# Kernel tuning notes

Measured on AMD Instinct MI355X. Metric: run time of the kernel, lower is better.

Reference implementation:

```python
import jax, jax.numpy as jnp
import numpy as np

N = 50000          # nodes
E = 800000         # edges (before self-loops)
F_IN = 128         # num_features
HEADS = 4
OUT = 128 // HEADS # per-head channels = num_hidden // heads
NEG_SLOPE = 0.2    # PyG GATConv default


def setup_inputs() -> dict:
    key = jax.random.key(0)
    ks = jax.random.split(key, 10)
    x = jax.random.normal(ks[0], (N, F_IN), jnp.float32)
    edge_index = jax.random.randint(ks[1], (2, E), 0, N, dtype=jnp.int64)
    sW = 1.0 / np.sqrt(F_IN)
    sA = 1.0 / np.sqrt(OUT)
    return {
        "x": x,
        "edge_index": edge_index,
        "W1": jax.random.normal(ks[2], (F_IN, HEADS * OUT), jnp.float32) * sW,
        "a_src1": jax.random.normal(ks[3], (HEADS, OUT), jnp.float32) * sA,
        "a_dst1": jax.random.normal(ks[4], (HEADS, OUT), jnp.float32) * sA,
        "b1": jnp.zeros((HEADS * OUT,), jnp.float32),
        "W2": jax.random.normal(ks[5], (HEADS * OUT, HEADS * OUT), jnp.float32) * sW,
        "a_src2": jax.random.normal(ks[6], (HEADS, OUT), jnp.float32) * sA,
        "a_dst2": jax.random.normal(ks[7], (HEADS, OUT), jnp.float32) * sA,
        "b2": jnp.zeros((HEADS * OUT,), jnp.float32),
    }


def gat_conv(x, src, dst, W, a_src, a_dst, b):
    """One GATConv layer (PyG semantics, concat heads, self-loops already in src/dst)."""
    n = x.shape[0]
    h = (x @ W).reshape(n, HEADS, OUT)                 # [N, H, C]
    # per-node attention halves, gathered per edge -> [Etot, H]
    alpha = (h * a_src).sum(-1)[src] + (h * a_dst).sum(-1)[dst]
    alpha = jax.nn.leaky_relu(alpha, NEG_SLOPE)
    # softmax over incoming edges of each destination node (stable)
    amax = jax.ops.segment_max(alpha, dst, num_segments=n)
    ex = jnp.exp(alpha - amax[dst])
    denom = jax.ops.segment_sum(ex, dst, num_segments=n)
    attn = ex / (denom[dst] + 1e-16)                    # [Etot, H]
    # weighted message scatter-add
    out = jax.ops.segment_sum(h[src] * attn[..., None], dst, num_segments=n)
    return out.reshape(n, HEADS * OUT) + b


def reference(x, edge_index, W1, a_src1, a_dst1, b1, W2, a_src2, a_dst2, b2):
    loops = jnp.arange(N, dtype=edge_index.dtype)       # PyG add_self_loops=True
    src = jnp.concatenate([edge_index[0], loops])
    dst = jnp.concatenate([edge_index[1], loops])
    h = jax.nn.relu(gat_conv(x, src, dst, W1, a_src1, a_dst1, b1))
    # dropout = identity in eval mode
    h = jax.nn.relu(gat_conv(h, src, dst, W2, a_src2, a_dst2, b2))
    return h
```

## Files before the change

kernel.cpp:

```cpp
#include <hip/hip_runtime.h>
#include <hip/hip_fp16.h>
#include <cstdint>
#include <cstddef>

#define NN 50000
#define EE 800000
#define ETOT (EE + NN)
#define FD 128
#define NH 4
#define NEG_SLOPE 0.2f

#define BSHIFT 10
#define BSIZE 1024
#define NBKT ((NN + BSIZE - 1) / BSIZE)
#define CAPG 20000
#define CHUNK 2048
#define P1_BLOCKS ((ETOT + CHUNK - 1) / CHUNK)

typedef _Float16 half8 __attribute__((ext_vector_type(8)));
typedef float f32x4 __attribute__((ext_vector_type(4)));


__global__ void zero_kernel(int* __restrict__ gcnt) {
    int t = threadIdx.x;
    if (t < NBKT) gcnt[t] = 0;
}


__global__ __launch_bounds__(256) void bin_kernel(const int* __restrict__ ei,
                                                  int* __restrict__ gcnt,
                                                  uint32_t* __restrict__ gbkt,
                                                  const float* __restrict__ W1,
                                                  const float* __restrict__ W2,
                                                  uint4* __restrict__ Wf1,
                                                  uint4* __restrict__ Wf2) {
    if (blockIdx.x >= P1_BLOCKS) {
        const float* W = (blockIdx.x - P1_BLOCKS) ? W2 : W1;
        uint4* Wf = (blockIdx.x - P1_BLOCKS) ? Wf2 : Wf1;
        for (int s = threadIdx.x; s < 2048; s += 256) {
            int fi = s >> 6;
            int lane = s & 63;
            int ct = fi >> 2, ks = fi & 3;
            int col = ct * 16 + (lane & 15);
            int kb = ks * 32 + (lane >> 4) * 8;
            half8 h;
            #pragma unroll
            for (int j = 0; j < 8; ++j) h[j] = (_Float16)W[(kb + j) * FD + col];
            Wf[s] = *(uint4*)&h;
        }
        return;
    }
    __shared__ int lcnt[NBKT];
    __shared__ int gb[NBKT];
    const int t = threadIdx.x;
    if (t < NBKT) lcnt[t] = 0;
    __syncthreads();
    const int base = blockIdx.x * CHUNK;
    uint32_t pk[8]; int bk[8]; int sl[8];
    #pragma unroll
    for (int j = 0; j < 8; ++j) {
        int e = base + j * 256 + t;
        bk[j] = -1;
        if (e < ETOT) {
            int src, dst;
            if (e < EE) { src = ei[e]; dst = ei[EE + e]; }
            else        { src = e - EE; dst = src; }
            int b = dst >> BSHIFT;
            bk[j] = b;
            pk[j] = (uint32_t)src | ((uint32_t)(dst & (BSIZE - 1)) << 16);
            sl[j] = atomicAdd(&lcnt[b], 1);
        }
    }
    __syncthreads();
    if (t < NBKT) gb[t] = atomicAdd(&gcnt[t], lcnt[t]);
    __syncthreads();
    #pragma unroll
    for (int j = 0; j < 8; ++j)
        if (bk[j] >= 0)
            gbkt[(size_t)bk[j] * CAPG + gb[bk[j]] + sl[j]] = pk[j];
}


__global__ __launch_bounds__(1024) void sort_kernel(const int* __restrict__ gcnt,
                                                    const uint32_t* __restrict__ gbkt,
                                                    int* __restrict__ row_ptr,
                                                    int* __restrict__ csr) {
    __shared__ int cnt[BSIZE];
    __shared__ int pfx[BSIZE];
    __shared__ int wsum[16];
    __shared__ int sCbase;
    const int b = blockIdx.x;
    const int t = threadIdx.x;
    const int count = gcnt[b];
    const int dstBase = b << BSHIFT;
    const int ndst = (NN - dstBase < BSIZE) ? (NN - dstBase) : BSIZE;
    const uint32_t* mybkt = gbkt + (size_t)b * CAPG;
    cnt[t] = 0;
    if (t < 64) {
        int v = (t < NBKT) ? gcnt[t] : 0;
        int inc = v;
        #pragma unroll
        for (int off = 1; off < 64; off <<= 1) {
            int u = __shfl_up(inc, off);
            if (t >= off) inc += u;
        }
        if (t == b) sCbase = inc - v;
    }
    __syncthreads();
    const int cbase = sCbase;
    for (int i = t; i < count; i += 1024)
        atomicAdd(&cnt[mybkt[i] >> 16], 1);
    __syncthreads();
    int v = cnt[t];
    int inc = v;
    const int lane = t & 63, wid = t >> 6;
    #pragma unroll
    for (int off = 1; off < 64; off <<= 1) {
        int u = __shfl_up(inc, off);
        if (lane >= off) inc += u;
    }
    if (lane == 63) wsum[wid] = inc;
    __syncthreads();
    if (t < 16) {
        int w = wsum[t]; int wi = w;
        #pragma unroll
        for (int off = 1; off < 16; off <<= 1) {
            int u = __shfl_up(wi, off);
            if (t >= off) wi += u;
        }
        wsum[t] = wi - w;
    }
    __syncthreads();
    int excl = wsum[wid] + inc - v;
    pfx[t] = excl;
    if (t < ndst) row_ptr[dstBase + t] = cbase + excl;
    if (b == NBKT - 1 && t == 0) row_ptr[NN] = ETOT;
    cnt[t] = 0;
    __syncthreads();
    for (int i = t; i < count; i += 1024) {
        uint32_t pkv = mybkt[i];
        int dl = pkv >> 16;
        int r = atomicAdd(&cnt[dl], 1);
        csr[cbase + pfx[dl] + r] = (int)(pkv & 0xFFFFu);
    }
}


__global__ __launch_bounds__(256) void gemm_kernel(const float* __restrict__ X,
                                                   const uint4* __restrict__ Wf,
                                                   __half* __restrict__ Hh) {
    const int tid = threadIdx.x;
    const int wv = tid >> 6, lane = tid & 63;
    const int l15 = lane & 15, lg = lane >> 4;
    const int rowA = blockIdx.x * 64 + wv * 16 + l15;
    const int rA = (rowA < NN) ? rowA : NN - 1;
    half8 a[4];
    #pragma unroll
    for (int ks = 0; ks < 4; ++ks) {
        int kb = ks * 32 + lg * 8;
        float4 x0 = *(const float4*)&X[(size_t)rA * FD + kb];
        float4 x1 = *(const float4*)&X[(size_t)rA * FD + kb + 4];
        a[ks][0] = (_Float16)x0.x; a[ks][1] = (_Float16)x0.y;
        a[ks][2] = (_Float16)x0.z; a[ks][3] = (_Float16)x0.w;
        a[ks][4] = (_Float16)x1.x; a[ks][5] = (_Float16)x1.y;
        a[ks][6] = (_Float16)x1.z; a[ks][7] = (_Float16)x1.w;
    }
    const int rowC = blockIdx.x * 64 + wv * 16 + lg * 4;
    #pragma unroll
    for (int ct = 0; ct < 8; ++ct) {
        uint4 braw[4];
        #pragma unroll
        for (int ks = 0; ks < 4; ++ks) braw[ks] = Wf[(ct * 4 + ks) * 64 + lane];
        f32x4 acc = {0.f, 0.f, 0.f, 0.f};
        #pragma unroll
        for (int ks = 0; ks < 4; ++ks) {
            half8 b = *(half8*)&braw[ks];
            acc = __builtin_amdgcn_mfma_f32_16x16x32_f16(a[ks], b, acc, 0, 0, 0);
        }
        #pragma unroll
        for (int r = 0; r < 4; ++r) {
            int gr = rowC + r;
            if (gr < NN) Hh[(size_t)gr * FD + ct * 16 + l15] = __float2half(acc[r]);
        }
    }
}


__global__ __launch_bounds__(256) void adot_kernel(const __half* __restrict__ H,
                                                   const float* __restrict__ a_src,
                                                   const float* __restrict__ a_dst,
                                                   float* __restrict__ AS,
                                                   float* __restrict__ AD) {
    int gt = blockIdx.x * 256 + threadIdx.x;
    int n = gt >> 4;
    int l = gt & 15;
    if (n >= NN) return;
    union { uint4 u; __half2 q[4]; } hv;
    hv.u = *(const uint4*)&H[(size_t)n * FD + l * 8];
    float ps = 0.f, pd = 0.f;
    #pragma unroll
    for (int j = 0; j < 4; ++j) {
        float2 f = __half22float2(hv.q[j]);
        ps += f.x * a_src[l * 8 + 2 * j] + f.y * a_src[l * 8 + 2 * j + 1];
        pd += f.x * a_dst[l * 8 + 2 * j] + f.y * a_dst[l * 8 + 2 * j + 1];
    }
    ps += __shfl_xor(ps, 1); ps += __shfl_xor(ps, 2);
    pd += __shfl_xor(pd, 1); pd += __shfl_xor(pd, 2);
    if ((l & 3) == 0) {
        AS[n * NH + (l >> 2)] = ps;
        AD[n * NH + (l >> 2)] = pd;
    }
}


__device__ __forceinline__ float sel4(float a0, float a1, float a2, float a3, int h) {
    float lo = (h & 1) ? a1 : a0;
    float hi = (h & 1) ? a3 : a2;
    return (h & 2) ? hi : lo;
}

__global__ __launch_bounds__(256) void agg_kernel(const __half* __restrict__ H,
                                                  const float* __restrict__ AS,
                                                  const float* __restrict__ AD,
                                                  const int* __restrict__ row_ptr,
                                                  const int* __restrict__ csr_src,
                                                  const float* __restrict__ bias,
                                                  float* __restrict__ Out) {
    __shared__ float sP[8][32][5];
    __shared__ int   sS[8][32];
    const int wave = threadIdx.x >> 6;
    const int lane = threadIdx.x & 63;
    const int sub  = lane >> 5;
    const int sl   = lane & 31;
    const int ws   = wave * 2 + sub;
    const int n = blockIdx.x * 8 + ws;
    const int start = row_ptr[n], end = row_ptr[n + 1];
    const int h0 = sl >> 3;
    const float4 adv = *(const float4*)&AD[n * NH];
    float s[NH] = {0.f, 0.f, 0.f, 0.f};
    float acc0 = 0.f, acc1 = 0.f, acc2 = 0.f, acc3 = 0.f;

    for (int base = start; base < end; base += 32) {
        int cn = end - base; if (cn > 32) cn = 32;
        int my_src = 0;
        float al[NH];
        if (sl < cn) {
            my_src = csr_src[base + sl];
            float4 asv = *(const float4*)&AS[my_src * NH];
            al[0] = asv.x + adv.x; al[1] = asv.y + adv.y;
            al[2] = asv.z + adv.z; al[3] = asv.w + adv.w;
        }
        sS[ws][sl] = my_src;
        #pragma unroll
        for (int h = 0; h < NH; ++h) {
            float aa = al[h];
            aa = (aa > 0.f) ? aa : NEG_SLOPE * aa;
            float pp = (sl < cn) ? __expf(aa) : 0.f;
            sP[ws][sl][h] = pp;
            #pragma unroll
            for (int off = 16; off; off >>= 1) pp += __shfl_xor(pp, off, 32);
            s[h] += pp;
        }
        #pragma unroll 4
        for (int e = 0; e < cn; ++e) {
            float pm = sP[ws][e][h0];
            int se = sS[ws][e];
            union { uint2 u; __half2 q[2]; } hv;
            hv.u = *(const uint2*)&H[(size_t)se * FD + sl * 4];
            float2 f0 = __half22float2(hv.q[0]);
            float2 f1 = __half22float2(hv.q[1]);
            acc0 += pm * f0.x; acc1 += pm * f0.y;
            acc2 += pm * f1.x; acc3 += pm * f1.y;
        }
    }
    float sh = sel4(s[0], s[1], s[2], s[3], h0);
    float inv = 1.f / (sh + 1e-16f);
    const float4 bv = *(const float4*)&bias[sl * 4];
    float4 ov;
    ov.x = fmaxf(acc0 * inv + bv.x, 0.f);
    ov.y = fmaxf(acc1 * inv + bv.y, 0.f);
    ov.z = fmaxf(acc2 * inv + bv.z, 0.f);
    ov.w = fmaxf(acc3 * inv + bv.w, 0.f);
    *(float4*)&Out[(size_t)n * FD + sl * 4] = ov;
}


extern "C" void kernel_launch(void* const* d_in, const int* in_sizes, int n_in,
                              void* d_out, int out_size, void* d_ws, size_t ws_size,
                              hipStream_t stream) {
    const float* x     = (const float*)d_in[0];
    const int*   ei    = (const int*)d_in[1];
    const float* W1    = (const float*)d_in[2];
    const float* asrc1 = (const float*)d_in[3];
    const float* adst1 = (const float*)d_in[4];
    const float* b1    = (const float*)d_in[5];
    const float* W2    = (const float*)d_in[6];
    const float* asrc2 = (const float*)d_in[7];
    const float* adst2 = (const float*)d_in[8];
    const float* b2    = (const float*)d_in[9];
    float* out = (float*)d_out;

    char* p = (char*)d_ws;
    auto alloc = [&](size_t bytes) {
        char* q = p;
        p += (bytes + 255) & ~(size_t)255;
        return q;
    };
    int*      row_ptr = (int*)alloc((NN + 1) * sizeof(int));
    int*      gcnt    = (int*)alloc(NBKT * sizeof(int));
    uint32_t* gbkt    = (uint32_t*)alloc((size_t)NBKT * CAPG * sizeof(uint32_t));
    int*      csr     = (int*)alloc((size_t)ETOT * sizeof(int));
    float*    AS      = (float*)alloc((size_t)NN * NH * sizeof(float));
    float*    AD      = (float*)alloc((size_t)NN * NH * sizeof(float));
    __half*   Hh      = (__half*)alloc((size_t)NN * FD * sizeof(__half));
    uint4*    Wf1     = (uint4*)alloc(2048 * sizeof(uint4));
    uint4*    Wf2     = (uint4*)alloc(2048 * sizeof(uint4));
    (void)ws_size; (void)in_sizes; (void)n_in; (void)out_size;

    zero_kernel<<<1, 64, 0, stream>>>(gcnt);
    bin_kernel<<<P1_BLOCKS + 2, 256, 0, stream>>>(ei, gcnt, gbkt, W1, W2, Wf1, Wf2);
    sort_kernel<<<NBKT, 1024, 0, stream>>>(gcnt, gbkt, row_ptr, csr);

    gemm_kernel<<<(NN + 63) / 64, 256, 0, stream>>>(x, Wf1, Hh);
    adot_kernel<<<(NN * 16 + 255) / 256, 256, 0, stream>>>(Hh, asrc1, adst1, AS, AD);
    agg_kernel<<<NN / 8, 256, 0, stream>>>(Hh, AS, AD, row_ptr, csr, b1, out);

    gemm_kernel<<<(NN + 63) / 64, 256, 0, stream>>>(out, Wf2, Hh);
    adot_kernel<<<(NN * 16 + 255) / 256, 256, 0, stream>>>(Hh, asrc2, adst2, AS, AD);
    agg_kernel<<<NN / 8, 256, 0, stream>>>(Hh, AS, AD, row_ptr, csr, b2, out);
}
```

Before: 150.3 us.

## Process four edges per wave concurrently with 16-byte feature loads in aggregation

The aggregation kernel now assigns one full 64-lane wave per destination node instead of a half-wave. Lanes are split into four edge slots of 16 lanes, and each lane loads 8 half-precision channels (16 bytes) per edge. Partial sums are combined across edge slots with cross-lane shuffles at the end. The intent is more memory-level parallelism and wider loads in the gather loop. The cost is extra shuffle reductions, idle lanes at low-degree tails, and half as many nodes per block.

```diff
diff --git a/kernel.cpp b/kernel.cpp
--- a/kernel.cpp
+++ b/kernel.cpp
@@ -213,12 +213,6 @@
 }
 
 
-__device__ __forceinline__ float sel4(float a0, float a1, float a2, float a3, int h) {
-    float lo = (h & 1) ? a1 : a0;
-    float hi = (h & 1) ? a3 : a2;
-    return (h & 2) ? hi : lo;
-}
-
 __global__ __launch_bounds__(256) void agg_kernel(const __half* __restrict__ H,
                                                   const float* __restrict__ AS,
                                                   const float* __restrict__ AD,
@@ -226,62 +220,77 @@
                                                   const int* __restrict__ csr_src,
                                                   const float* __restrict__ bias,
                                                   float* __restrict__ Out) {
-    __shared__ float sP[8][32][5];
-    __shared__ int   sS[8][32];
-    const int wave = threadIdx.x >> 6;
+    __shared__ float sP[4][64][5];
+    __shared__ int   sS[4][64];
+    const int wv   = threadIdx.x >> 6;
     const int lane = threadIdx.x & 63;
-    const int sub  = lane >> 5;
-    const int sl   = lane & 31;
-    const int ws   = wave * 2 + sub;
-    const int n = blockIdx.x * 8 + ws;
+    const int n = blockIdx.x * 4 + wv;
     const int start = row_ptr[n], end = row_ptr[n + 1];
-    const int h0 = sl >> 3;
+    const int eslot = lane >> 4;
+    const int c8    = lane & 15;
+    const int hme   = c8 >> 2;
     const float4 adv = *(const float4*)&AD[n * NH];
     float s[NH] = {0.f, 0.f, 0.f, 0.f};
-    float acc0 = 0.f, acc1 = 0.f, acc2 = 0.f, acc3 = 0.f;
-
-    for (int base = start; base < end; base += 32) {
-        int cn = end - base; if (cn > 32) cn = 32;
+    float acc[8] = {0.f, 0.f, 0.f, 0.f, 0.f, 0.f, 0.f, 0.f};
+
+    for (int base = start; base < end; base += 64) {
+        int cn = end - base; if (cn > 64) cn = 64;
         int my_src = 0;
         float al[NH];
-        if (sl < cn) {
-            my_src = csr_src[base + sl];
+        if (lane < cn) {
+            my_src = csr_src[base + lane];
             float4 asv = *(const float4*)&AS[my_src * NH];
             al[0] = asv.x + adv.x; al[1] = asv.y + adv.y;
             al[2] = asv.z + adv.z; al[3] = asv.w + adv.w;
         }
-        sS[ws][sl] = my_src;
+        sS[wv][lane] = my_src;
         #pragma unroll
         for (int h = 0; h < NH; ++h) {
             float aa = al[h];
             aa = (aa > 0.f) ? aa : NEG_SLOPE * aa;
-            float pp = (sl < cn) ? __expf(aa) : 0.f;
-            sP[ws][sl][h] = pp;
+            float pp = (lane < cn) ? __expf(aa) : 0.f;
+            sP[wv][lane][h] = pp;
             #pragma unroll
-            for (int off = 16; off; off >>= 1) pp += __shfl_xor(pp, off, 32);
+            for (int off = 32; off; off >>= 1) pp += __shfl_xor(pp, off);
             s[h] += pp;
         }
-        #pragma unroll 4
-        for (int e = 0; e < cn; ++e) {
-            float pm = sP[ws][e][h0];
-            int se = sS[ws][e];
-            union { uint2 u; __half2 q[2]; } hv;
-            hv.u = *(const uint2*)&H[(size_t)se * FD + sl * 4];
-            float2 f0 = __half22float2(hv.q[0]);
-            float2 f1 = __half22float2(hv.q[1]);
-            acc0 += pm * f0.x; acc1 += pm * f0.y;
-            acc2 += pm * f1.x; acc3 += pm * f1.y;
-        }
-    }
-    float sh = sel4(s[0], s[1], s[2], s[3], h0);
-    float inv = 1.f / (sh + 1e-16f);
-    const float4 bv = *(const float4*)&bias[sl * 4];
-    float4 ov;
-    ov.x = fmaxf(acc0 * inv + bv.x, 0.f);
-    ov.y = fmaxf(acc1 * inv + bv.y, 0.f);
-    ov.z = fmaxf(acc2 * inv + bv.z, 0.f);
-    ov.w = fmaxf(acc3 * inv + bv.w, 0.f);
-    *(float4*)&Out[(size_t)n * FD + sl * 4] = ov;
+        #pragma unroll 2
+        for (int cb = 0; cb < cn; cb += 4) {
+            int e = cb + eslot;
+            if (e < cn) {
+                int   se = sS[wv][e];
+                float pm = sP[wv][e][hme];
+                union { uint4 u; __half2 q[4]; } hv;
+                hv.u = *(const uint4*)&H[(size_t)se * FD + c8 * 8];
+                #pragma unroll
+                for (int j = 0; j < 4; ++j) {
+                    float2 f = __half22float2(hv.q[j]);
+                    acc[2 * j]     += pm * f.x;
+                    acc[2 * j + 1] += pm * f.y;
+                }
+            }
+        }
+    }
+    #pragma unroll
+    for (int m = 16; m <= 32; m <<= 1)
+        #pragma unroll
+        for (int j = 0; j < 8; ++j) acc[j] += __shfl_xor(acc[j], m);
+    if (eslot == 0) {
+        float inv = 1.f / (s[hme] + 1e-16f);
+        float4 b0 = *(const float4*)&bias[c8 * 8];
+        float4 b1 = *(const float4*)&bias[c8 * 8 + 4];
+        float4 o0, o1;
+        o0.x = fmaxf(acc[0] * inv + b0.x, 0.f);
+        o0.y = fmaxf(acc[1] * inv + b0.y, 0.f);
+        o0.z = fmaxf(acc[2] * inv + b0.z, 0.f);
+        o0.w = fmaxf(acc[3] * inv + b0.w, 0.f);
+        o1.x = fmaxf(acc[4] * inv + b1.x, 0.f);
+        o1.y = fmaxf(acc[5] * inv + b1.y, 0.f);
+        o1.z = fmaxf(acc[6] * inv + b1.z, 0.f);
+        o1.w = fmaxf(acc[7] * inv + b1.w, 0.f);
+        *(float4*)&Out[(size_t)n * FD + c8 * 8]     = o0;
+        *(float4*)&Out[(size_t)n * FD + c8 * 8 + 4] = o1;
+    }
 }
 
 
@@ -323,9 +332,9 @@
 
     gemm_kernel<<<(NN + 63) / 64, 256, 0, stream>>>(x, Wf1, Hh);
     adot_kernel<<<(NN * 16 + 255) / 256, 256, 0, stream>>>(Hh, asrc1, adst1, AS, AD);
-    agg_kernel<<<NN / 8, 256, 0, stream>>>(Hh, AS, AD, row_ptr, csr, b1, out);
+    agg_kernel<<<NN / 4, 256, 0, stream>>>(Hh, AS, AD, row_ptr, csr, b1, out);
 
     gemm_kernel<<<(NN + 63) / 64, 256, 0, stream>>>(out, Wf2, Hh);
     adot_kernel<<<(NN * 16 + 255) / 256, 256, 0, stream>>>(Hh, asrc2, adst2, AS, AD);
-    agg_kernel<<<NN / 8, 256, 0, stream>>>(Hh, AS, AD, row_ptr, csr, b2, out);
-}
+    agg_kernel<<<NN / 4, 256, 0, stream>>>(Hh, AS, AD, row_ptr, csr, b2, out);
+}
```

After: 167.8 us. 1.12x slower.
